# Performance work log

Hardware: AMD Instinct MI355X
Metric: run time of the kernel (lower is better)

Reference implementation:

```python
import jax, jax.numpy as jnp
import numpy as np

LRELU_SLOPE = 0.2  # PyG GATConv default negative_slope
LN_EPS = 1e-5


def _layer_norm(x, g, b):
    mu = x.mean(-1, keepdims=True)
    var = x.var(-1, keepdims=True)
    return (x - mu) / jnp.sqrt(var + LN_EPS) * g + b


def _gat_conv(x, src, dst, W, a_src, a_dst, bias, heads, out_c, concat):
    # PyG GATConv (eval mode, self-loops already appended to src/dst).
    N = x.shape[0]
    h = (x @ W).reshape(N, heads, out_c)            # [N,H,C]
    e_src = (h * a_src).sum(-1)                     # [N,H]
    e_dst = (h * a_dst).sum(-1)                     # [N,H]
    e = jax.nn.leaky_relu(e_src[src] + e_dst[dst], LRELU_SLOPE)  # [E,H]
    # segment softmax over incoming edges of each dst node
    m = jax.ops.segment_max(e, dst, num_segments=N)
    m = jnp.where(jnp.isfinite(m), m, 0.0)
    w = jnp.exp(e - m[dst])
    denom = jax.ops.segment_sum(w, dst, num_segments=N)
    alpha = w / (denom[dst] + 1e-16)                # [E,H]
    out = jax.ops.segment_sum(h[src] * alpha[:, :, None], dst, num_segments=N)  # [N,H,C]
    out = out.reshape(N, heads * out_c) if concat else out.mean(1)
    return out + bias


def setup_inputs() -> dict:
    key = jax.random.key(0)
    ks = jax.random.split(key, 16)
    N, E, F0, Hd, H, G = 50000, 800000, 32, 32, 4, 512
    s = 0.1
    nrm = lambda k, shape: jax.random.normal(k, shape, jnp.float32) * s
    d = {}
    d['x'] = jax.random.normal(ks[0], (N, F0), jnp.float32)
    d['edge_index'] = jax.random.randint(ks[1], (2, E), 0, N)
    d['batch'] = jnp.sort(jax.random.randint(ks[2], (N,), 0, G))
    d['num_graphs'] = G
    # layer 1: F0 -> (Hd, H heads, concat)
    d['W1'] = nrm(ks[3], (F0, H * Hd)); d['as1'] = nrm(ks[4], (H, Hd)); d['ad1'] = nrm(ks[5], (H, Hd))
    d['b1'] = jnp.zeros((H * Hd,)); d['g1'] = jnp.ones((H * Hd,)); d['be1'] = jnp.zeros((H * Hd,))
    # layer 2: H*Hd -> (Hd, H heads, concat)
    d['W2'] = nrm(ks[6], (H * Hd, H * Hd)); d['as2'] = nrm(ks[7], (H, Hd)); d['ad2'] = nrm(ks[8], (H, Hd))
    d['b2'] = jnp.zeros((H * Hd,)); d['g2'] = jnp.ones((H * Hd,)); d['be2'] = jnp.zeros((H * Hd,))
    # layer 3: H*Hd -> (Hd, 1 head, mean)
    d['W3'] = nrm(ks[9], (H * Hd, Hd)); d['as3'] = nrm(ks[10], (1, Hd)); d['ad3'] = nrm(ks[11], (1, Hd))
    d['b3'] = jnp.zeros((Hd,)); d['g3'] = jnp.ones((Hd,)); d['be3'] = jnp.zeros((Hd,))
    # classifier MLP: 2*Hd -> Hd -> Hd//2 -> 1 (torch Linear [out,in])
    d['cW1'] = nrm(ks[12], (Hd, 2 * Hd)); d['cb1'] = jnp.zeros((Hd,))
    d['cW2'] = nrm(ks[13], (Hd // 2, Hd)); d['cb2'] = jnp.zeros((Hd // 2,))
    d['cW3'] = nrm(ks[14], (1, Hd // 2)); d['cb3'] = jnp.zeros((1,))
    return d


def reference(x, edge_index, batch, num_graphs,
              W1, as1, ad1, b1, g1, be1,
              W2, as2, ad2, b2, g2, be2,
              W3, as3, ad3, b3, g3, be3,
              cW1, cb1, cW2, cb2, cW3, cb3):
    N = x.shape[0]
    loop = jnp.arange(N)
    src = jnp.concatenate([edge_index[0], loop])
    dst = jnp.concatenate([edge_index[1], loop])
    h = jax.nn.elu(_layer_norm(_gat_conv(x, src, dst, W1, as1, ad1, b1, 4, 32, True), g1, be1))
    h = jax.nn.elu(_layer_norm(_gat_conv(h, src, dst, W2, as2, ad2, b2, 4, 32, True), g2, be2))
    h = jax.nn.elu(_layer_norm(_gat_conv(h, src, dst, W3, as3, ad3, b3, 1, 32, False), g3, be3))
    cnt = jax.ops.segment_sum(jnp.ones((N,), h.dtype), batch, num_segments=num_graphs)
    x_mean = jax.ops.segment_sum(h, batch, num_segments=num_graphs) / jnp.maximum(cnt, 1.0)[:, None]
    x_max = jax.ops.segment_max(h, batch, num_segments=num_graphs)
    f = jnp.concatenate([x_mean, x_max], axis=1)        # [G, 64]
    f = jax.nn.relu(f @ cW1.T + cb1)
    f = jax.nn.relu(f @ cW2.T + cb2)
    return (f @ cW3.T + cb3).squeeze(-1)                 # [G]
```

## Files before the change

kernel.cpp:

```cpp
#include <hip/hip_runtime.h>
#include <hip/hip_fp16.h>
#include <math.h>

#define CDIV(a, b) (((a) + (b) - 1) / (b))
#define SCAN_BS 1024
#define NBUK 512
#define ATILE 4096

typedef _Float16 f16x8 __attribute__((ext_vector_type(8)));
typedef float f32x4 __attribute__((ext_vector_type(4)));

__device__ __forceinline__ unsigned encf(float v) {
    unsigned u = __float_as_uint(v);
    return (u & 0x80000000u) ? ~u : (u | 0x80000000u);
}
__device__ __forceinline__ float decf(unsigned k) {
    unsigned u = (k & 0x80000000u) ? (k ^ 0x80000000u) : ~k;
    return __uint_as_float(u);
}

__device__ __forceinline__ float lrelu(float v) {
    return v > 0.f ? v : 0.2f * v;
}

__global__ __launch_bounds__(256) void gemm_kernel(
    const float* __restrict__ X, const float* __restrict__ W,
    float* __restrict__ Y, int M, int K, int Nout) {
    int idx = blockIdx.x * blockDim.x + threadIdx.x;
    if (idx >= M * Nout) return;
    int row = idx / Nout;
    int col = idx - row * Nout;
    const float* xr = X + (size_t)row * K;
    const float* wc = W + col;
    float acc = 0.f;
    for (int k = 0; k < K; k += 4) {
        float4 xv = *(const float4*)(xr + k);
        acc += xv.x * wc[(size_t)(k + 0) * Nout];
        acc += xv.y * wc[(size_t)(k + 1) * Nout];
        acc += xv.z * wc[(size_t)(k + 2) * Nout];
        acc += xv.w * wc[(size_t)(k + 3) * Nout];
    }
    Y[idx] = acc;
}

__global__ __launch_bounds__(256) void wprep_kernel(
    const float* __restrict__ W, __half* __restrict__ Whf, int K, int NOUT) {
    int NK = K / 32, NT = NOUT / 16;
    int tot = NT * NK * 64;
    int idx = blockIdx.x * blockDim.x + threadIdx.x;
    if (idx >= tot) return;
    int l = idx & 63, f = idx >> 6;
    int ks = f % NK, t = f / NK;
    int quad = l >> 4, c15 = l & 15;
    _Float16 v[8];
#pragma unroll
    for (int j = 0; j < 8; ++j) {
        int k = ks * 32 + quad * 8 + j;
        int n = t * 16 + c15;
        v[j] = (_Float16)W[(size_t)k * NOUT + n];
    }
    *(uint4*)(Whf + (size_t)idx * 8) = *(uint4*)v;
}

__device__ __forceinline__ f16x8 loadA(const float* p) {
    float4 lo = *(const float4*)p;
    float4 hi = *(const float4*)(p + 4);
    f16x8 a;
    a[0] = (_Float16)lo.x; a[1] = (_Float16)lo.y;
    a[2] = (_Float16)lo.z; a[3] = (_Float16)lo.w;
    a[4] = (_Float16)hi.x; a[5] = (_Float16)hi.y;
    a[6] = (_Float16)hi.z; a[7] = (_Float16)hi.w;
    return a;
}
__device__ __forceinline__ f16x8 loadA(const __half* p) {
    return *(const f16x8*)p;
}

template <int K, int NOUT, typename XT>
__global__ __launch_bounds__(256) void gemm_mfma(
    const XT* __restrict__ X, const __half* __restrict__ Whf,
    __half* __restrict__ Y, int M) {
    constexpr int NK = K / 32, NT = NOUT / 16;
    int wave = threadIdx.x >> 6, lane = threadIdx.x & 63;
    int quad = lane >> 4, c15 = lane & 15;
    int row0 = (blockIdx.x * 4 + wave) * 16;
    if (row0 >= M) return;
    int arow = row0 + c15;
    if (arow >= M) arow = M - 1;
    const XT* xr = X + (size_t)arow * K + quad * 8;
    const f16x8* bp = (const f16x8*)Whf;
    f32x4 acc[NT];
#pragma unroll
    for (int t = 0; t < NT; ++t) {
        acc[t][0] = 0.f; acc[t][1] = 0.f; acc[t][2] = 0.f; acc[t][3] = 0.f;
    }
#pragma unroll
    for (int ks = 0; ks < NK; ++ks) {
        f16x8 a = loadA(xr + ks * 32);
#pragma unroll
        for (int t = 0; t < NT; ++t) {
            f16x8 b = bp[(t * NK + ks) * 64 + lane];
            acc[t] = __builtin_amdgcn_mfma_f32_16x16x32_f16(a, b, acc[t],
                                                            0, 0, 0);
        }
    }
#pragma unroll
    for (int r = 0; r < 4; ++r) {
        int row = row0 + quad * 4 + r;
        if (row < M) {
#pragma unroll
            for (int t = 0; t < NT; ++t)
                Y[(size_t)row * NOUT + t * 16 + c15] = (__half)acc[t][r];
        }
    }
}

__global__ __launch_bounds__(256) void attn16_kernel(
    const __half* __restrict__ h, const float* __restrict__ a_src,
    const float* __restrict__ a_dst, float* __restrict__ es,
    float* __restrict__ ed, int N, int H) {
    int idx = blockIdx.x * blockDim.x + threadIdx.x;
    if (idx >= N * H) return;
    int n = idx / H;
    int hh = idx - n * H;
    const __half* hp = h + (size_t)n * H * 32 + hh * 32;
    const float* ap = a_src + hh * 32;
    const float* bp = a_dst + hh * 32;
    float s = 0.f, d = 0.f;
#pragma unroll
    for (int c = 0; c < 32; c += 2) {
        float2 f = __half22float2(*(const __half2*)(hp + c));
        s += f.x * ap[c] + f.y * ap[c + 1];
        d += f.x * bp[c] + f.y * bp[c + 1];
    }
    es[idx] = s;
    ed[idx] = d;
}

__global__ __launch_bounds__(256) void attn_kernel(
    const float* __restrict__ h, const float* __restrict__ a_src,
    const float* __restrict__ a_dst, float* __restrict__ es,
    float* __restrict__ ed, int N, int H, int C) {
    int idx = blockIdx.x * blockDim.x + threadIdx.x;
    if (idx >= N * H) return;
    int n = idx / H;
    int hh = idx - n * H;
    const float* hp = h + (size_t)n * H * C + (size_t)hh * C;
    const float* ap = a_src + hh * C;
    const float* bp = a_dst + hh * C;
    float s = 0.f, d = 0.f;
    for (int c = 0; c < C; c += 4) {
        float4 hv = *(const float4*)(hp + c);
        float4 av = *(const float4*)(ap + c);
        float4 bv = *(const float4*)(bp + c);
        s += hv.x * av.x + hv.y * av.y + hv.z * av.z + hv.w * av.w;
        d += hv.x * bv.x + hv.y * bv.y + hv.z * bv.z + hv.w * bv.w;
    }
    es[idx] = s;
    ed[idx] = d;
}

__global__ __launch_bounds__(256) void binA1_kernel(
    const int* __restrict__ ei, int E, int* __restrict__ ghist) {
    __shared__ int lh[NBUK];
    int t = threadIdx.x;
    for (int i = t; i < NBUK; i += 256) lh[i] = 0;
    __syncthreads();
    int base = blockIdx.x * ATILE;
#pragma unroll 4
    for (int j = 0; j < ATILE / 256; ++j) {
        int idx = base + t + 256 * j;
        if (idx < E) atomicAdd(&lh[ei[E + idx] >> 7], 1);
    }
    __syncthreads();
    int* gh = ghist + (size_t)blockIdx.x * NBUK;
    for (int i = t; i < NBUK; i += 256) gh[i] = lh[i];
}

__global__ __launch_bounds__(64) void binA2a_kernel(
    int* __restrict__ ghist, int* __restrict__ tot, int nblk) {
    int b = blockIdx.x;
    int lane = threadIdx.x;
    int accb = 0;
    for (int chunk = 0; chunk < nblk; chunk += 64) {
        int i = chunk + lane;
        int v = (i < nblk) ? ghist[(size_t)i * NBUK + b] : 0;
        int s = v;
        for (int off = 1; off < 64; off <<= 1) {
            int tv = __shfl_up(s, off);
            if (lane >= off) s += tv;
        }
        if (i < nblk) ghist[(size_t)i * NBUK + b] = s - v + accb;
        accb += __shfl(s, 63);
    }
    if (lane == 0) tot[b] = accb;
}

__global__ __launch_bounds__(NBUK) void binA2b_kernel(
    const int* __restrict__ tot, int* __restrict__ bucketptr,
    int* __restrict__ rowptr, int N, int E) {
    __shared__ int sc[NBUK];
    int b = threadIdx.x;
    int v = tot[b];
    sc[b] = v;
    __syncthreads();
    for (int off = 1; off < NBUK; off <<= 1) {
        int t = (b >= off) ? sc[b - off] : 0;
        __syncthreads();
        sc[b] += t;
        __syncthreads();
    }
    bucketptr[b] = sc[b] - v;
    if (b == 0) {
        bucketptr[NBUK] = E;
        rowptr[N] = E + N;
    }
}

__global__ __launch_bounds__(256) void binA3_kernel(
    const int* __restrict__ ei, int E, const int* __restrict__ ghist,
    const int* __restrict__ bucketptr, unsigned* __restrict__ ebuf) {
    __shared__ int lcur[NBUK];
    int t = threadIdx.x;
    const int* gh = ghist + (size_t)blockIdx.x * NBUK;
    for (int i = t; i < NBUK; i += 256) lcur[i] = gh[i] + bucketptr[i];
    __syncthreads();
    int base = blockIdx.x * ATILE;
#pragma unroll 4
    for (int j = 0; j < ATILE / 256; ++j) {
        int idx = base + t + 256 * j;
        if (idx < E) {
            int s = ei[idx];
            int d = ei[E + idx];
            int pos = atomicAdd(&lcur[d >> 7], 1);
            ebuf[pos] = ((unsigned)d << 16) | (unsigned)s;
        }
    }
}

__global__ __launch_bounds__(256) void binB_kernel(
    const unsigned* __restrict__ ebuf, const int* __restrict__ bucketptr,
    int* __restrict__ rowptr, int* __restrict__ csrc, int N) {
    __shared__ int cnt_[128];
    __shared__ int pre[128];
    __shared__ int lcur[128];
    int b = blockIdx.x;
    int t = threadIdx.x;
    int n0 = b << 7;
    if (t < 128) cnt_[t] = 0;
    __syncthreads();
    int beg = bucketptr[b], end = bucketptr[b + 1];
    for (int i = beg + t; i < end; i += 256)
        atomicAdd(&cnt_[(ebuf[i] >> 16) - n0], 1);
    __syncthreads();
    if (t < 128) pre[t] = (n0 + t < N) ? (cnt_[t] + 1) : 0;
    __syncthreads();
    for (int off = 1; off < 128; off <<= 1) {
        int v = 0;
        if (t < 128 && t >= off) v = pre[t - off];
        __syncthreads();
        if (t < 128) pre[t] += v;
        __syncthreads();
    }
    int cbase = beg + n0;
    if (t < 128 && n0 + t < N) {
        int excl = pre[t] - (cnt_[t] + 1);
        int rp = cbase + excl;
        rowptr[n0 + t] = rp;
        csrc[rp] = n0 + t;
        lcur[t] = rp + 1;
    }
    __syncthreads();
    for (int i = beg + t; i < end; i += 256) {
        unsigned e = ebuf[i];
        int d = (int)(e >> 16) - n0;
        int s = (int)(e & 0xFFFFu);
        int pos = atomicAdd(&lcur[d], 1);
        csrc[pos] = s;
    }
}

__global__ __launch_bounds__(256) void deg_kernel(const int* __restrict__ ei,
                                                  int E,
                                                  int* __restrict__ deg) {
    int e = blockIdx.x * blockDim.x + threadIdx.x;
    if (e >= E) return;
    atomicAdd(&deg[ei[E + e]], 1);
}

__global__ __launch_bounds__(SCAN_BS) void scan1_kernel(
    const int* __restrict__ deg, int* __restrict__ rowptr,
    int* __restrict__ bsum, int N) {
    __shared__ int tmp[SCAN_BS];
    int tid = threadIdx.x;
    int gid = blockIdx.x * SCAN_BS + tid;
    int v = (gid < N) ? (deg[gid] + 1) : 0;
    tmp[tid] = v;
    __syncthreads();
    for (int off = 1; off < SCAN_BS; off <<= 1) {
        int t = (tid >= off) ? tmp[tid - off] : 0;
        __syncthreads();
        tmp[tid] += t;
        __syncthreads();
    }
    if (gid < N) rowptr[gid] = tmp[tid] - v;
    if (tid == SCAN_BS - 1) bsum[blockIdx.x] = tmp[tid];
}

__global__ void scan2_kernel(int* __restrict__ bsum, int nb) {
    if (threadIdx.x == 0 && blockIdx.x == 0) {
        int acc = 0;
        for (int i = 0; i < nb; ++i) {
            int t = bsum[i];
            bsum[i] = acc;
            acc += t;
        }
    }
}

__global__ __launch_bounds__(SCAN_BS) void scan3_kernel(
    int* __restrict__ rowptr, int* __restrict__ cursor,
    int* __restrict__ csrc, const int* __restrict__ bsum, int N, int total) {
    int gid = blockIdx.x * SCAN_BS + threadIdx.x;
    if (gid < N) {
        int v = rowptr[gid] + bsum[blockIdx.x];
        rowptr[gid] = v;
        cursor[gid] = v + 1;
        csrc[v] = gid;
    }
    if (gid == 0) rowptr[N] = total;
}

__global__ __launch_bounds__(256) void scatter_kernel(
    const int* __restrict__ ei, int E, int* __restrict__ cursor,
    int* __restrict__ csrc) {
    int e = blockIdx.x * blockDim.x + threadIdx.x;
    if (e >= E) return;
    int s = ei[e];
    int d = ei[E + e];
    int pos = atomicAdd(&cursor[d], 1);
    csrc[pos] = s;
}

__global__ __launch_bounds__(256) void aggr_ln128_kernel(
    const int* __restrict__ rowptr, const int* __restrict__ csrc,
    const __half* __restrict__ h, const float* __restrict__ es,
    const float* __restrict__ ed, const float* __restrict__ bias,
    const float* __restrict__ gam, const float* __restrict__ bet,
    __half* __restrict__ outp, int N) {
    constexpr int D = 128, H = 4;
    int wave = (blockIdx.x * blockDim.x + threadIdx.x) >> 6;
    int lane = threadIdx.x & 63;
    int grp = lane >> 5;
    int li = lane & 31;
    int d = wave * 2 + grp;
    if (d >= N) return;
    int c = li * 4;
    int hh = li >> 3;
    float edv = ed[d * H + hh];
    float l = 0.f;
    float ax = 0.f, ay = 0.f, az = 0.f, aw = 0.f;
    int k = rowptr[d], end = rowptr[d + 1];
    for (; k + 8 <= end; k += 8) {
        int s[8];
#pragma unroll
        for (int j = 0; j < 8; ++j) s[j] = csrc[k + j];
        float e[8];
#pragma unroll
        for (int j = 0; j < 8; ++j) e[j] = es[s[j] * H + hh];
        uint2 u[8];
#pragma unroll
        for (int j = 0; j < 8; ++j)
            u[j] = *(const uint2*)(h + (size_t)s[j] * D + c);
#pragma unroll
        for (int j = 0; j < 8; ++j) {
            float w = __expf(lrelu(e[j] + edv));
            float2 f0 = __half22float2(*(__half2*)&u[j].x);
            float2 f1 = __half22float2(*(__half2*)&u[j].y);
            l += w;
            ax += w * f0.x; ay += w * f0.y; az += w * f1.x; aw += w * f1.y;
        }
    }
    for (; k + 4 <= end; k += 4) {
        int s[4];
#pragma unroll
        for (int j = 0; j < 4; ++j) s[j] = csrc[k + j];
        float e[4];
#pragma unroll
        for (int j = 0; j < 4; ++j) e[j] = es[s[j] * H + hh];
        uint2 u[4];
#pragma unroll
        for (int j = 0; j < 4; ++j)
            u[j] = *(const uint2*)(h + (size_t)s[j] * D + c);
#pragma unroll
        for (int j = 0; j < 4; ++j) {
            float w = __expf(lrelu(e[j] + edv));
            float2 f0 = __half22float2(*(__half2*)&u[j].x);
            float2 f1 = __half22float2(*(__half2*)&u[j].y);
            l += w;
            ax += w * f0.x; ay += w * f0.y; az += w * f1.x; aw += w * f1.y;
        }
    }
    for (; k < end; ++k) {
        int s = csrc[k];
        float w = __expf(lrelu(es[s * H + hh] + edv));
        uint2 u = *(const uint2*)(h + (size_t)s * D + c);
        float2 f0 = __half22float2(*(__half2*)&u.x);
        float2 f1 = __half22float2(*(__half2*)&u.y);
        l += w;
        ax += w * f0.x; ay += w * f0.y; az += w * f1.x; aw += w * f1.y;
    }
    float rl = 1.f / (l + 1e-16f);
    float4 b4 = *(const float4*)(bias + c);
    float v0 = ax * rl + b4.x;
    float v1 = ay * rl + b4.y;
    float v2 = az * rl + b4.z;
    float v3 = aw * rl + b4.w;
    float s = v0 + v1 + v2 + v3;
    float ss = v0 * v0 + v1 * v1 + v2 * v2 + v3 * v3;
    for (int off = 16; off; off >>= 1) {
        s += __shfl_xor(s, off);
        ss += __shfl_xor(ss, off);
    }
    float mean = s / D;
    float var = ss / D - mean * mean;
    float rstd = rsqrtf(var + 1e-5f);
    float4 g4 = *(const float4*)(gam + c);
    float4 t4 = *(const float4*)(bet + c);
    float4 o;
    o.x = (v0 - mean) * rstd * g4.x + t4.x;
    o.y = (v1 - mean) * rstd * g4.y + t4.y;
    o.z = (v2 - mean) * rstd * g4.z + t4.z;
    o.w = (v3 - mean) * rstd * g4.w + t4.w;
    o.x = o.x > 0.f ? o.x : expm1f(o.x);
    o.y = o.y > 0.f ? o.y : expm1f(o.y);
    o.z = o.z > 0.f ? o.z : expm1f(o.z);
    o.w = o.w > 0.f ? o.w : expm1f(o.w);
    __half2 p0 = __floats2half2_rn(o.x, o.y);
    __half2 p1 = __floats2half2_rn(o.z, o.w);
    uint2 u;
    u.x = *(unsigned*)&p0;
    u.y = *(unsigned*)&p1;
    *(uint2*)(outp + (size_t)d * D + c) = u;
}

__global__ __launch_bounds__(256) void aggr_ln32_pool_kernel(
    const int* __restrict__ rowptr, const int* __restrict__ csrc,
    const __half* __restrict__ h, const float* __restrict__ es,
    const float* __restrict__ ed, const float* __restrict__ bias,
    const float* __restrict__ gam, const float* __restrict__ bet,
    const int* __restrict__ batch, float* __restrict__ psum,
    unsigned* __restrict__ pmax, float* __restrict__ cnt, int N) {
    constexpr int D = 32;
    __shared__ float lsum[2][32];
    __shared__ unsigned lmax[2][32];
    __shared__ float lcnt[2];
    __shared__ int g0s;
    int tid = threadIdx.x;
    int wave = (blockIdx.x * blockDim.x + tid) >> 6;
    int lane = tid & 63;
    int half = lane >> 5;
    int c = lane & 31;
    int d = wave * 2 + half;
    int dbase = blockIdx.x * 8;
    if (tid < 64) {
        lsum[tid >> 5][tid & 31] = 0.f;
        lmax[tid >> 5][tid & 31] = 0u;
    }
    if (tid < 2) lcnt[tid] = 0.f;
    if (tid == 0) g0s = batch[dbase < N ? dbase : (N - 1)];
    __syncthreads();
    int g0 = g0s;
    bool active = d < N;
    if (active) {
        float edv = ed[d];
        float l = 0.f, acc = 0.f;
        int k = rowptr[d], end = rowptr[d + 1];
        for (; k + 8 <= end; k += 8) {
            int s[8];
#pragma unroll
            for (int j = 0; j < 8; ++j) s[j] = csrc[k + j];
            float e[8];
#pragma unroll
            for (int j = 0; j < 8; ++j) e[j] = es[s[j]];
            float hv[8];
#pragma unroll
            for (int j = 0; j < 8; ++j)
                hv[j] = __half2float(h[(size_t)s[j] * D + c]);
#pragma unroll
            for (int j = 0; j < 8; ++j) {
                float w = __expf(lrelu(e[j] + edv));
                l += w;
                acc += w * hv[j];
            }
        }
        for (; k + 4 <= end; k += 4) {
            int s[4];
#pragma unroll
            for (int j = 0; j < 4; ++j) s[j] = csrc[k + j];
            float e[4];
#pragma unroll
            for (int j = 0; j < 4; ++j) e[j] = es[s[j]];
            float hv[4];
#pragma unroll
            for (int j = 0; j < 4; ++j)
                hv[j] = __half2float(h[(size_t)s[j] * D + c]);
#pragma unroll
            for (int j = 0; j < 4; ++j) {
                float w = __expf(lrelu(e[j] + edv));
                l += w;
                acc += w * hv[j];
            }
        }
        for (; k < end; ++k) {
            int s = csrc[k];
            float w = __expf(lrelu(es[s] + edv));
            l += w;
            acc += w * __half2float(h[(size_t)s * D + c]);
        }
        float v = acc / (l + 1e-16f) + bias[c];
        float sm = v, ss = v * v;
        for (int off = 16; off; off >>= 1) {
            sm += __shfl_xor(sm, off);
            ss += __shfl_xor(ss, off);
        }
        float mean = sm / D;
        float var = ss / D - mean * mean;
        float rstd = rsqrtf(var + 1e-5f);
        float o = (v - mean) * rstd * gam[c] + bet[c];
        o = o > 0.f ? o : expm1f(o);
        int g = batch[d];
        int goff = g - g0;
        if (goff >= 0 && goff < 2) {
            atomicAdd(&lsum[goff][c], o);
            atomicMax(&lmax[goff][c], encf(o));
            if (c == 0) atomicAdd(&lcnt[goff], 1.0f);
        } else {
            atomicAdd(&psum[g * D + c], o);
            atomicMax(&pmax[g * D + c], encf(o));
            if (c == 0) atomicAdd(&cnt[g], 1.0f);
        }
    }
    __syncthreads();
    if (tid < 64) {
        int go = tid >> 5, cc = tid & 31;
        unsigned m = lmax[go][cc];
        if (m != 0u) {
            int gg = g0 + go;
            atomicAdd(&psum[gg * D + cc], lsum[go][cc]);
            atomicMax(&pmax[gg * D + cc], m);
            if (cc == 0) atomicAdd(&cnt[gg], lcnt[go]);
        }
    }
}

__global__ __launch_bounds__(256) void aggr_csr_kernel(
    const int* __restrict__ rowptr, const int* __restrict__ csrc,
    const float* __restrict__ h, const float* __restrict__ es,
    const float* __restrict__ ed, float* __restrict__ outp, int N, int H,
    int C) {
    int D = H * C;
    int wave = (blockIdx.x * blockDim.x + threadIdx.x) >> 6;
    int lane = threadIdx.x & 63;
    if (wave >= N) return;
    int d = wave;
    int c0 = lane, c1 = lane + 64;
    bool a0 = c0 < D, a1 = c1 < D;
    int h0 = a0 ? c0 / C : 0;
    int h1 = a1 ? c1 / C : 0;
    float edv0 = a0 ? ed[d * H + h0] : 0.f;
    float edv1 = a1 ? ed[d * H + h1] : 0.f;
    float m0 = -INFINITY, m1 = -INFINITY;
    float l0 = 0.f, l1 = 0.f, acc0 = 0.f, acc1 = 0.f;
    int beg = rowptr[d], end = rowptr[d + 1];
    for (int k = beg; k < end; ++k) {
        int s = csrc[k];
        const float* hp = h + (size_t)s * D;
        if (a0) {
            float v = lrelu(es[s * H + h0] + edv0);
            float nm = fmaxf(m0, v);
            float sc = __expf(m0 - nm);
            float w = __expf(v - nm);
            l0 = l0 * sc + w;
            acc0 = acc0 * sc + w * hp[c0];
            m0 = nm;
        }
        if (a1) {
            float v = lrelu(es[s * H + h1] + edv1);
            float nm = fmaxf(m1, v);
            float sc = __expf(m1 - nm);
            float w = __expf(v - nm);
            l1 = l1 * sc + w;
            acc1 = acc1 * sc + w * hp[c1];
            m1 = nm;
        }
    }
    if (a0) outp[(size_t)d * D + c0] = acc0 / (l0 + 1e-16f);
    if (a1) outp[(size_t)d * D + c1] = acc1 / (l1 + 1e-16f);
}

__global__ __launch_bounds__(64) void ln_elu_kernel(
    const float* __restrict__ in, const float* __restrict__ bias,
    const float* __restrict__ gam, const float* __restrict__ bet,
    float* __restrict__ outp, int D) {
    int n = blockIdx.x;
    int lane = threadIdx.x;
    int c0 = lane, c1 = lane + 64;
    bool a0 = c0 < D, a1 = c1 < D;
    float v0 = 0.f, v1 = 0.f;
    if (a0) v0 = in[(size_t)n * D + c0] + bias[c0];
    if (a1) v1 = in[(size_t)n * D + c1] + bias[c1];
    float s = v0 + v1;
    float ss = v0 * v0 + v1 * v1;
    for (int off = 32; off; off >>= 1) {
        s += __shfl_xor(s, off);
        ss += __shfl_xor(ss, off);
    }
    float mean = s / D;
    float var = ss / D - mean * mean;
    float rstd = rsqrtf(var + 1e-5f);
    if (a0) {
        float o = (v0 - mean) * rstd * gam[c0] + bet[c0];
        outp[(size_t)n * D + c0] = o > 0.f ? o : expm1f(o);
    }
    if (a1) {
        float o = (v1 - mean) * rstd * gam[c1] + bet[c1];
        outp[(size_t)n * D + c1] = o > 0.f ? o : expm1f(o);
    }
}

__global__ __launch_bounds__(256) void pool_kernel(
    const float* __restrict__ h, const int* __restrict__ batch, int N, int C,
    float* __restrict__ psum, unsigned* __restrict__ pmax,
    float* __restrict__ cnt) {
    int idx = blockIdx.x * blockDim.x + threadIdx.x;
    if (idx >= N * C) return;
    int n = idx / C;
    int c = idx - n * C;
    int g = batch[n];
    float v = h[(size_t)n * C + c];
    atomicAdd(&psum[g * C + c], v);
    atomicMax(&pmax[g * C + c], encf(v));
    if (c == 0) atomicAdd(&cnt[g], 1.0f);
}

__global__ __launch_bounds__(64) void mlp_kernel(
    const float* __restrict__ psum, const unsigned* __restrict__ pmax,
    const float* __restrict__ cnt, const float* __restrict__ cW1,
    const float* __restrict__ cb1, const float* __restrict__ cW2,
    const float* __restrict__ cb2, const float* __restrict__ cW3,
    const float* __restrict__ cb3, float* __restrict__ outp, int C) {
    __shared__ float f[64];
    __shared__ float t1[32];
    __shared__ float t2[16];
    int g = blockIdx.x;
    int t = threadIdx.x;
    float c = fmaxf(cnt[g], 1.0f);
    if (t < C) {
        f[t] = psum[g * C + t] / c;
    } else if (t < 2 * C) {
        unsigned k = pmax[g * C + (t - C)];
        f[t] = (k == 0u) ? -INFINITY : decf(k);
    }
    __syncthreads();
    if (t < 32) {
        float a = cb1[t];
        for (int i = 0; i < 64; ++i) a += f[i] * cW1[t * 64 + i];
        t1[t] = fmaxf(a, 0.f);
    }
    __syncthreads();
    if (t < 16) {
        float a = cb2[t];
        for (int i = 0; i < 32; ++i) a += t1[i] * cW2[t * 32 + i];
        t2[t] = fmaxf(a, 0.f);
    }
    __syncthreads();
    if (t == 0) {
        float a = cb3[0];
        for (int i = 0; i < 16; ++i) a += t2[i] * cW3[i];
        outp[g] = a;
    }
}

extern "C" void kernel_launch(void* const* d_in, const int* in_sizes, int n_in,
                              void* d_out, int out_size, void* d_ws,
                              size_t ws_size, hipStream_t stream) {
    const float* x = (const float*)d_in[0];
    const int* ei = (const int*)d_in[1];
    const int* batch = (const int*)d_in[2];
    const float* W1 = (const float*)d_in[4];
    const float* as1 = (const float*)d_in[5];
    const float* ad1 = (const float*)d_in[6];
    const float* b1 = (const float*)d_in[7];
    const float* g1 = (const float*)d_in[8];
    const float* be1 = (const float*)d_in[9];
    const float* W2 = (const float*)d_in[10];
    const float* as2 = (const float*)d_in[11];
    const float* ad2 = (const float*)d_in[12];
    const float* b2 = (const float*)d_in[13];
    const float* g2 = (const float*)d_in[14];
    const float* be2 = (const float*)d_in[15];
    const float* W3 = (const float*)d_in[16];
    const float* as3 = (const float*)d_in[17];
    const float* ad3 = (const float*)d_in[18];
    const float* b3 = (const float*)d_in[19];
    const float* g3 = (const float*)d_in[20];
    const float* be3 = (const float*)d_in[21];
    const float* cW1 = (const float*)d_in[22];
    const float* cb1 = (const float*)d_in[23];
    const float* cW2 = (const float*)d_in[24];
    const float* cb2 = (const float*)d_in[25];
    const float* cW3 = (const float*)d_in[26];
    const float* cb3 = (const float*)d_in[27];

    const int N = in_sizes[2];
    const int E = in_sizes[1] / 2;
    const int F0 = in_sizes[0] / N;
    const int Hd = in_sizes[19];
    const int H = in_sizes[5] / Hd;
    const int D = H * Hd;
    const int H3 = in_sizes[17] / Hd;
    const int G = out_size;
    const int EN = E + N;
    const bool shapes_ok = (F0 == 32 && Hd == 32 && H == 4 && D == 128 &&
                            H3 == 1 && N <= 65536);

    char* w = (char*)d_ws;
    size_t off = 0;
    auto carve = [&](size_t bytes) -> void* {
        void* p = w + off;
        off = (off + bytes + 255) & ~(size_t)255;
        return p;
    };
    float* Q = (float*)carve((size_t)N * D * 4);
    __half* Qh = (__half*)Q;
    float* R = (float*)carve((size_t)N * D * 4);
    float* P = (float*)carve((size_t)N * D * 4);
    __half* Ph = (__half*)P;
    float* es = (float*)carve((size_t)N * H * 4);
    float* ed = (float*)carve((size_t)N * H * 4);
    int* rowptr = (int*)carve((size_t)(N + 1) * 4);
    int* cursor = (int*)carve((size_t)N * 4);
    int* csrc = (int*)carve((size_t)EN * 4);
    int* bsum = (int*)carve((size_t)CDIV(N, SCAN_BS) * 4);
    const int nblkA = CDIV(E, ATILE);
    int* ghist = (int*)carve((size_t)nblkA * NBUK * 4);
    int* tot = (int*)carve((size_t)NBUK * 4);
    int* bucketptr = (int*)carve((size_t)(NBUK + 1) * 4);
    unsigned* ebuf = (unsigned*)carve((size_t)E * 4);
    __half* wh1 = (__half*)carve((size_t)8 * 1 * 64 * 8 * 2);
    __half* wh2 = (__half*)carve((size_t)8 * 4 * 64 * 8 * 2);
    __half* wh3 = (__half*)carve((size_t)2 * 4 * 64 * 8 * 2);
    float* psum = (float*)carve((size_t)G * Hd * 4);
    unsigned* pmax = (unsigned*)carve((size_t)G * Hd * 4);
    float* cnt = (float*)carve((size_t)G * 4);
    (void)ws_size;
    (void)n_in;

    const int BLK = 256;
    const int nb = CDIV(N, SCAN_BS);

    hipMemsetAsync(psum, 0, (size_t)G * Hd * 4, stream);
    hipMemsetAsync(pmax, 0, (size_t)G * Hd * 4, stream);
    hipMemsetAsync(cnt, 0, (size_t)G * 4, stream);

    if (shapes_ok) {
        binA1_kernel<<<nblkA, 256, 0, stream>>>(ei, E, ghist);
        binA2a_kernel<<<NBUK, 64, 0, stream>>>(ghist, tot, nblkA);
        binA2b_kernel<<<1, NBUK, 0, stream>>>(tot, bucketptr, rowptr, N, E);
        binA3_kernel<<<nblkA, 256, 0, stream>>>(ei, E, ghist, bucketptr, ebuf);
        binB_kernel<<<CDIV(N, 128), 256, 0, stream>>>(ebuf, bucketptr, rowptr,
                                                      csrc, N);
        wprep_kernel<<<CDIV(8 * 1 * 64, BLK), BLK, 0, stream>>>(W1, wh1, 32, 128);
        wprep_kernel<<<CDIV(8 * 4 * 64, BLK), BLK, 0, stream>>>(W2, wh2, 128, 128);
        wprep_kernel<<<CDIV(2 * 4 * 64, BLK), BLK, 0, stream>>>(W3, wh3, 128, 32);
        gemm_mfma<32, 128, float><<<CDIV(N, 64), 256, 0, stream>>>(x, wh1, Qh, N);
        attn16_kernel<<<CDIV(N * 4, BLK), BLK, 0, stream>>>(Qh, as1, ad1, es, ed, N, 4);
        aggr_ln128_kernel<<<CDIV(N, 8), 256, 0, stream>>>(
            rowptr, csrc, Qh, es, ed, b1, g1, be1, Ph, N);
        gemm_mfma<128, 128, __half><<<CDIV(N, 64), 256, 0, stream>>>(Ph, wh2, Qh, N);
        attn16_kernel<<<CDIV(N * 4, BLK), BLK, 0, stream>>>(Qh, as2, ad2, es, ed, N, 4);
        aggr_ln128_kernel<<<CDIV(N, 8), 256, 0, stream>>>(
            rowptr, csrc, Qh, es, ed, b2, g2, be2, Ph, N);
        gemm_mfma<128, 32, __half><<<CDIV(N, 64), 256, 0, stream>>>(Ph, wh3, Qh, N);
        attn16_kernel<<<CDIV(N, BLK), BLK, 0, stream>>>(Qh, as3, ad3, es, ed, N, 1);
        aggr_ln32_pool_kernel<<<CDIV(N, 8), 256, 0, stream>>>(
            rowptr, csrc, Qh, es, ed, b3, g3, be3, batch, psum, pmax, cnt, N);
    } else {
        hipMemsetAsync(cursor, 0, (size_t)N * 4, stream);
        deg_kernel<<<CDIV(E, BLK), BLK, 0, stream>>>(ei, E, cursor);
        scan1_kernel<<<nb, SCAN_BS, 0, stream>>>(cursor, rowptr, bsum, N);
        scan2_kernel<<<1, 64, 0, stream>>>(bsum, nb);
        scan3_kernel<<<nb, SCAN_BS, 0, stream>>>(rowptr, cursor, csrc, bsum, N, EN);
        scatter_kernel<<<CDIV(E, BLK), BLK, 0, stream>>>(ei, E, cursor, csrc);
        gemm_kernel<<<CDIV(N * D, BLK), BLK, 0, stream>>>(x, W1, Q, N, F0, D);
        attn_kernel<<<CDIV(N * H, BLK), BLK, 0, stream>>>(Q, as1, ad1, es, ed, N, H, Hd);
        aggr_csr_kernel<<<CDIV(N, 4), BLK, 0, stream>>>(rowptr, csrc, Q, es, ed, R, N, H, Hd);
        ln_elu_kernel<<<N, 64, 0, stream>>>(R, b1, g1, be1, P, D);
        gemm_kernel<<<CDIV(N * D, BLK), BLK, 0, stream>>>(P, W2, Q, N, D, D);
        attn_kernel<<<CDIV(N * H, BLK), BLK, 0, stream>>>(Q, as2, ad2, es, ed, N, H, Hd);
        aggr_csr_kernel<<<CDIV(N, 4), BLK, 0, stream>>>(rowptr, csrc, Q, es, ed, R, N, H, Hd);
        ln_elu_kernel<<<N, 64, 0, stream>>>(R, b2, g2, be2, P, D);
        gemm_kernel<<<CDIV(N * Hd, BLK), BLK, 0, stream>>>(P, W3, Q, N, D, Hd);
        attn_kernel<<<CDIV(N * H3, BLK), BLK, 0, stream>>>(Q, as3, ad3, es, ed, N, H3, Hd);
        aggr_csr_kernel<<<CDIV(N, 4), BLK, 0, stream>>>(rowptr, csrc, Q, es, ed, R, N, H3, Hd);
        ln_elu_kernel<<<N, 64, 0, stream>>>(R, b3, g3, be3, P, Hd);
        pool_kernel<<<CDIV(N * Hd, BLK), BLK, 0, stream>>>(P, batch, N, Hd, psum, pmax, cnt);
    }

    mlp_kernel<<<G, 64, 0, stream>>>(psum, pmax, cnt, cW1, cb1, cW2, cb2, cW3,
                                     cb3, (float*)d_out, Hd);
}
```

Baseline: 316.9 us.

## Fuse attention logits into MFMA GEMM and merge small setup kernels

The per-node attention score computation (es/ed) moves into the GEMM epilogue, using cross-lane shuffles on the accumulator registers. This drops three separate attention kernels and their re-read of the fp16 features. The single-block bucket scan is folded into binA3 and binB, which each recompute it, and the three weight-prep launches become one kernel. Zeroing of the pooling buffers moves into binA1 instead of three memsets, cutting launch count at the cost of some redundant per-block scan work and the assumption that psum/pmax/cnt are laid out contiguously.

```diff
diff --git a/kernel.cpp b/kernel.cpp
--- a/kernel.cpp
+++ b/kernel.cpp
@@ -43,23 +43,37 @@
     Y[idx] = acc;
 }
 
-__global__ __launch_bounds__(256) void wprep_kernel(
-    const float* __restrict__ W, __half* __restrict__ Whf, int K, int NOUT) {
-    int NK = K / 32, NT = NOUT / 16;
-    int tot = NT * NK * 64;
-    int idx = blockIdx.x * blockDim.x + threadIdx.x;
-    if (idx >= tot) return;
+__device__ __forceinline__ void wprep_one(const float* __restrict__ W,
+                                          __half* __restrict__ Whf, int K,
+                                          int NOUT, int idx) {
+    int NK = K / 32;
     int l = idx & 63, f = idx >> 6;
-    int ks = f % NK, t = f / NK;
+    int ks = f % NK, tt = f / NK;
     int quad = l >> 4, c15 = l & 15;
     _Float16 v[8];
 #pragma unroll
     for (int j = 0; j < 8; ++j) {
         int k = ks * 32 + quad * 8 + j;
-        int n = t * 16 + c15;
+        int n = tt * 16 + c15;
         v[j] = (_Float16)W[(size_t)k * NOUT + n];
     }
     *(uint4*)(Whf + (size_t)idx * 8) = *(uint4*)v;
+}
+
+__global__ __launch_bounds__(256) void wprep_all_kernel(
+    const float* __restrict__ W1, const float* __restrict__ W2,
+    const float* __restrict__ W3, __half* __restrict__ wh1,
+    __half* __restrict__ wh2, __half* __restrict__ wh3,
+    int* __restrict__ rowptr, int N, int E) {
+    int idx = blockIdx.x * 256 + threadIdx.x;
+    if (idx == 0) rowptr[N] = E + N;
+    if (idx < 512) {
+        wprep_one(W1, wh1, 32, 128, idx);
+    } else if (idx < 2560) {
+        wprep_one(W2, wh2, 128, 128, idx - 512);
+    } else if (idx < 3072) {
+        wprep_one(W3, wh3, 128, 32, idx - 2560);
+    }
 }
 
 __device__ __forceinline__ f16x8 loadA(const float* p) {
@@ -76,11 +90,14 @@
     return *(const f16x8*)p;
 }
 
-template <int K, int NOUT, typename XT>
-__global__ __launch_bounds__(256) void gemm_mfma(
+template <int K, int NOUT, int HH, typename XT>
+__global__ __launch_bounds__(256) void gemm_mfma_attn(
     const XT* __restrict__ X, const __half* __restrict__ Whf,
-    __half* __restrict__ Y, int M) {
+    __half* __restrict__ Y, const float* __restrict__ a_src,
+    const float* __restrict__ a_dst, float* __restrict__ es,
+    float* __restrict__ ed, int M) {
     constexpr int NK = K / 32, NT = NOUT / 16;
+    static_assert(NT == 2 * HH, "32 channels per head assumed");
     int wave = threadIdx.x >> 6, lane = threadIdx.x & 63;
     int quad = lane >> 4, c15 = lane & 15;
     int row0 = (blockIdx.x * 4 + wave) * 16;
@@ -113,28 +130,162 @@
                 Y[(size_t)row * NOUT + t * 16 + c15] = (__half)acc[t][r];
         }
     }
-}
-
-__global__ __launch_bounds__(256) void attn16_kernel(
-    const __half* __restrict__ h, const float* __restrict__ a_src,
-    const float* __restrict__ a_dst, float* __restrict__ es,
-    float* __restrict__ ed, int N, int H) {
-    int idx = blockIdx.x * blockDim.x + threadIdx.x;
-    if (idx >= N * H) return;
-    int n = idx / H;
-    int hh = idx - n * H;
-    const __half* hp = h + (size_t)n * H * 32 + hh * 32;
-    const float* ap = a_src + hh * 32;
-    const float* bp = a_dst + hh * 32;
-    float s = 0.f, d = 0.f;
-#pragma unroll
-    for (int c = 0; c < 32; c += 2) {
-        float2 f = __half22float2(*(const __half2*)(hp + c));
-        s += f.x * ap[c] + f.y * ap[c + 1];
-        d += f.x * bp[c] + f.y * bp[c + 1];
-    }
-    es[idx] = s;
-    ed[idx] = d;
+    float asv[NT], adv[NT];
+#pragma unroll
+    for (int t = 0; t < NT; ++t) {
+        asv[t] = a_src[t * 16 + c15];
+        adv[t] = a_dst[t * 16 + c15];
+    }
+#pragma unroll
+    for (int h = 0; h < HH; ++h) {
+#pragma unroll
+        for (int r = 0; r < 4; ++r) {
+            float s = acc[2 * h][r] * asv[2 * h] +
+                      acc[2 * h + 1][r] * asv[2 * h + 1];
+            float dd = acc[2 * h][r] * adv[2 * h] +
+                       acc[2 * h + 1][r] * adv[2 * h + 1];
+#pragma unroll
+            for (int off = 8; off >= 1; off >>= 1) {
+                s += __shfl_xor(s, off);
+                dd += __shfl_xor(dd, off);
+            }
+            int row = row0 + quad * 4 + r;
+            if (row < M) {
+                if (c15 == 0) es[row * HH + h] = s;
+                if (c15 == 1) ed[row * HH + h] = dd;
+            }
+        }
+    }
+}
+
+__global__ __launch_bounds__(256) void binA1_kernel(
+    const int* __restrict__ ei, int E, int* __restrict__ ghist,
+    int* __restrict__ pool0, int poolN) {
+    __shared__ int lh[NBUK];
+    int t = threadIdx.x;
+    int gid = blockIdx.x * 256 + t;
+    if (gid < poolN) pool0[gid] = 0;
+    for (int i = t; i < NBUK; i += 256) lh[i] = 0;
+    __syncthreads();
+    int base = blockIdx.x * ATILE;
+#pragma unroll 4
+    for (int j = 0; j < ATILE / 256; ++j) {
+        int idx = base + t + 256 * j;
+        if (idx < E) atomicAdd(&lh[ei[E + idx] >> 7], 1);
+    }
+    __syncthreads();
+    int* gh = ghist + (size_t)blockIdx.x * NBUK;
+    for (int i = t; i < NBUK; i += 256) gh[i] = lh[i];
+}
+
+__global__ __launch_bounds__(64) void binA2a_kernel(
+    int* __restrict__ ghist, int* __restrict__ tot, int nblk) {
+    int b = blockIdx.x;
+    int lane = threadIdx.x;
+    int accb = 0;
+    for (int chunk = 0; chunk < nblk; chunk += 64) {
+        int i = chunk + lane;
+        int v = (i < nblk) ? ghist[(size_t)i * NBUK + b] : 0;
+        int s = v;
+        for (int off = 1; off < 64; off <<= 1) {
+            int tv = __shfl_up(s, off);
+            if (lane >= off) s += tv;
+        }
+        if (i < nblk) ghist[(size_t)i * NBUK + b] = s - v + accb;
+        accb += __shfl(s, 63);
+    }
+    if (lane == 0) tot[b] = accb;
+}
+
+__device__ __forceinline__ void bucketScan(const int* __restrict__ tot,
+                                           int* __restrict__ sc, int t,
+                                           int& a0, int& a1, int& excl) {
+    a0 = tot[2 * t];
+    a1 = tot[2 * t + 1];
+    int pair = a0 + a1;
+    sc[t] = pair;
+    __syncthreads();
+#pragma unroll
+    for (int off = 1; off < 256; off <<= 1) {
+        int v = (t >= off) ? sc[t - off] : 0;
+        __syncthreads();
+        sc[t] += v;
+        __syncthreads();
+    }
+    excl = sc[t] - pair;
+}
+
+__global__ __launch_bounds__(256) void binA3_kernel(
+    const int* __restrict__ ei, int E, const int* __restrict__ ghist,
+    const int* __restrict__ tot, unsigned* __restrict__ ebuf) {
+    __shared__ int lcur[NBUK];
+    __shared__ int sc[256];
+    int t = threadIdx.x;
+    int a0, a1, excl;
+    bucketScan(tot, sc, t, a0, a1, excl);
+    const int* gh = ghist + (size_t)blockIdx.x * NBUK;
+    lcur[2 * t] = gh[2 * t] + excl;
+    lcur[2 * t + 1] = gh[2 * t + 1] + excl + a0;
+    __syncthreads();
+    int base = blockIdx.x * ATILE;
+#pragma unroll 4
+    for (int j = 0; j < ATILE / 256; ++j) {
+        int idx = base + t + 256 * j;
+        if (idx < E) {
+            int s = ei[idx];
+            int d = ei[E + idx];
+            int pos = atomicAdd(&lcur[d >> 7], 1);
+            ebuf[pos] = ((unsigned)d << 16) | (unsigned)s;
+        }
+    }
+}
+
+__global__ __launch_bounds__(256) void binB_kernel(
+    const unsigned* __restrict__ ebuf, const int* __restrict__ tot,
+    int* __restrict__ rowptr, int* __restrict__ csrc, int N) {
+    __shared__ int cnt_[128];
+    __shared__ int pre[128];
+    __shared__ int lcur[128];
+    __shared__ int sc[256];
+    __shared__ int begS;
+    int b = blockIdx.x;
+    int t = threadIdx.x;
+    int n0 = b << 7;
+    int totb = tot[b];
+    if (t < 128) cnt_[t] = 0;
+    int a0, a1, excl;
+    bucketScan(tot, sc, t, a0, a1, excl);
+    if (t == (b >> 1)) begS = (b & 1) ? (excl + a0) : excl;
+    __syncthreads();
+    int beg = begS, end = begS + totb;
+    for (int i = beg + t; i < end; i += 256)
+        atomicAdd(&cnt_[(ebuf[i] >> 16) - n0], 1);
+    __syncthreads();
+    if (t < 128) pre[t] = (n0 + t < N) ? (cnt_[t] + 1) : 0;
+    __syncthreads();
+    for (int off = 1; off < 128; off <<= 1) {
+        int v = 0;
+        if (t < 128 && t >= off) v = pre[t - off];
+        __syncthreads();
+        if (t < 128) pre[t] += v;
+        __syncthreads();
+    }
+    int cbase = beg + n0;
+    if (t < 128 && n0 + t < N) {
+        int ex = pre[t] - (cnt_[t] + 1);
+        int rp = cbase + ex;
+        rowptr[n0 + t] = rp;
+        csrc[rp] = n0 + t;
+        lcur[t] = rp + 1;
+    }
+    __syncthreads();
+    for (int i = beg + t; i < end; i += 256) {
+        unsigned e = ebuf[i];
+        int d = (int)(e >> 16) - n0;
+        int s = (int)(e & 0xFFFFu);
+        int pos = atomicAdd(&lcur[d], 1);
+        csrc[pos] = s;
+    }
 }
 
 __global__ __launch_bounds__(256) void attn_kernel(
@@ -158,126 +309,6 @@
     }
     es[idx] = s;
     ed[idx] = d;
-}
-
-__global__ __launch_bounds__(256) void binA1_kernel(
-    const int* __restrict__ ei, int E, int* __restrict__ ghist) {
-    __shared__ int lh[NBUK];
-    int t = threadIdx.x;
-    for (int i = t; i < NBUK; i += 256) lh[i] = 0;
-    __syncthreads();
-    int base = blockIdx.x * ATILE;
-#pragma unroll 4
-    for (int j = 0; j < ATILE / 256; ++j) {
-        int idx = base + t + 256 * j;
-        if (idx < E) atomicAdd(&lh[ei[E + idx] >> 7], 1);
-    }
-    __syncthreads();
-    int* gh = ghist + (size_t)blockIdx.x * NBUK;
-    for (int i = t; i < NBUK; i += 256) gh[i] = lh[i];
-}
-
-__global__ __launch_bounds__(64) void binA2a_kernel(
-    int* __restrict__ ghist, int* __restrict__ tot, int nblk) {
-    int b = blockIdx.x;
-    int lane = threadIdx.x;
-    int accb = 0;
-    for (int chunk = 0; chunk < nblk; chunk += 64) {
-        int i = chunk + lane;
-        int v = (i < nblk) ? ghist[(size_t)i * NBUK + b] : 0;
-        int s = v;
-        for (int off = 1; off < 64; off <<= 1) {
-            int tv = __shfl_up(s, off);
-            if (lane >= off) s += tv;
-        }
-        if (i < nblk) ghist[(size_t)i * NBUK + b] = s - v + accb;
-        accb += __shfl(s, 63);
-    }
-    if (lane == 0) tot[b] = accb;
-}
-
-__global__ __launch_bounds__(NBUK) void binA2b_kernel(
-    const int* __restrict__ tot, int* __restrict__ bucketptr,
-    int* __restrict__ rowptr, int N, int E) {
-    __shared__ int sc[NBUK];
-    int b = threadIdx.x;
-    int v = tot[b];
-    sc[b] = v;
-    __syncthreads();
-    for (int off = 1; off < NBUK; off <<= 1) {
-        int t = (b >= off) ? sc[b - off] : 0;
-        __syncthreads();
-        sc[b] += t;
-        __syncthreads();
-    }
-    bucketptr[b] = sc[b] - v;
-    if (b == 0) {
-        bucketptr[NBUK] = E;
-        rowptr[N] = E + N;
-    }
-}
-
-__global__ __launch_bounds__(256) void binA3_kernel(
-    const int* __restrict__ ei, int E, const int* __restrict__ ghist,
-    const int* __restrict__ bucketptr, unsigned* __restrict__ ebuf) {
-    __shared__ int lcur[NBUK];
-    int t = threadIdx.x;
-    const int* gh = ghist + (size_t)blockIdx.x * NBUK;
-    for (int i = t; i < NBUK; i += 256) lcur[i] = gh[i] + bucketptr[i];
-    __syncthreads();
-    int base = blockIdx.x * ATILE;
-#pragma unroll 4
-    for (int j = 0; j < ATILE / 256; ++j) {
-        int idx = base + t + 256 * j;
-        if (idx < E) {
-            int s = ei[idx];
-            int d = ei[E + idx];
-            int pos = atomicAdd(&lcur[d >> 7], 1);
-            ebuf[pos] = ((unsigned)d << 16) | (unsigned)s;
-        }
-    }
-}
-
-__global__ __launch_bounds__(256) void binB_kernel(
-    const unsigned* __restrict__ ebuf, const int* __restrict__ bucketptr,
-    int* __restrict__ rowptr, int* __restrict__ csrc, int N) {
-    __shared__ int cnt_[128];
-    __shared__ int pre[128];
-    __shared__ int lcur[128];
-    int b = blockIdx.x;
-    int t = threadIdx.x;
-    int n0 = b << 7;
-    if (t < 128) cnt_[t] = 0;
-    __syncthreads();
-    int beg = bucketptr[b], end = bucketptr[b + 1];
-    for (int i = beg + t; i < end; i += 256)
-        atomicAdd(&cnt_[(ebuf[i] >> 16) - n0], 1);
-    __syncthreads();
-    if (t < 128) pre[t] = (n0 + t < N) ? (cnt_[t] + 1) : 0;
-    __syncthreads();
-    for (int off = 1; off < 128; off <<= 1) {
-        int v = 0;
-        if (t < 128 && t >= off) v = pre[t - off];
-        __syncthreads();
-        if (t < 128) pre[t] += v;
-        __syncthreads();
-    }
-    int cbase = beg + n0;
-    if (t < 128 && n0 + t < N) {
-        int excl = pre[t] - (cnt_[t] + 1);
-        int rp = cbase + excl;
-        rowptr[n0 + t] = rp;
-        csrc[rp] = n0 + t;
-        lcur[t] = rp + 1;
-    }
-    __syncthreads();
-    for (int i = beg + t; i < end; i += 256) {
-        unsigned e = ebuf[i];
-        int d = (int)(e >> 16) - n0;
-        int s = (int)(e & 0xFFFFu);
-        int pos = atomicAdd(&lcur[d], 1);
-        csrc[pos] = s;
-    }
 }
 
 __global__ __launch_bounds__(256) void deg_kernel(const int* __restrict__ ei,
@@ -746,7 +777,6 @@
     const int nblkA = CDIV(E, ATILE);
     int* ghist = (int*)carve((size_t)nblkA * NBUK * 4);
     int* tot = (int*)carve((size_t)NBUK * 4);
-    int* bucketptr = (int*)carve((size_t)(NBUK + 1) * 4);
     unsigned* ebuf = (unsigned*)carve((size_t)E * 4);
     __half* wh1 = (__half*)carve((size_t)8 * 1 * 64 * 8 * 2);
     __half* wh2 = (__half*)carve((size_t)8 * 4 * 64 * 8 * 2);
@@ -759,34 +789,33 @@
 
     const int BLK = 256;
     const int nb = CDIV(N, SCAN_BS);
-
-    hipMemsetAsync(psum, 0, (size_t)G * Hd * 4, stream);
-    hipMemsetAsync(pmax, 0, (size_t)G * Hd * 4, stream);
-    hipMemsetAsync(cnt, 0, (size_t)G * 4, stream);
+    const int poolInts = G * Hd * 2 + G;
 
     if (shapes_ok) {
-        binA1_kernel<<<nblkA, 256, 0, stream>>>(ei, E, ghist);
+        binA1_kernel<<<nblkA, 256, 0, stream>>>(ei, E, ghist, (int*)psum,
+                                                poolInts);
         binA2a_kernel<<<NBUK, 64, 0, stream>>>(ghist, tot, nblkA);
-        binA2b_kernel<<<1, NBUK, 0, stream>>>(tot, bucketptr, rowptr, N, E);
-        binA3_kernel<<<nblkA, 256, 0, stream>>>(ei, E, ghist, bucketptr, ebuf);
-        binB_kernel<<<CDIV(N, 128), 256, 0, stream>>>(ebuf, bucketptr, rowptr,
+        binA3_kernel<<<nblkA, 256, 0, stream>>>(ei, E, ghist, tot, ebuf);
+        binB_kernel<<<CDIV(N, 128), 256, 0, stream>>>(ebuf, tot, rowptr,
                                                       csrc, N);
-        wprep_kernel<<<CDIV(8 * 1 * 64, BLK), BLK, 0, stream>>>(W1, wh1, 32, 128);
-        wprep_kernel<<<CDIV(8 * 4 * 64, BLK), BLK, 0, stream>>>(W2, wh2, 128, 128);
-        wprep_kernel<<<CDIV(2 * 4 * 64, BLK), BLK, 0, stream>>>(W3, wh3, 128, 32);
-        gemm_mfma<32, 128, float><<<CDIV(N, 64), 256, 0, stream>>>(x, wh1, Qh, N);
-        attn16_kernel<<<CDIV(N * 4, BLK), BLK, 0, stream>>>(Qh, as1, ad1, es, ed, N, 4);
+        wprep_all_kernel<<<12, 256, 0, stream>>>(W1, W2, W3, wh1, wh2, wh3,
+                                                 rowptr, N, E);
+        gemm_mfma_attn<32, 128, 4, float><<<CDIV(N, 64), 256, 0, stream>>>(
+            x, wh1, Qh, as1, ad1, es, ed, N);
         aggr_ln128_kernel<<<CDIV(N, 8), 256, 0, stream>>>(
             rowptr, csrc, Qh, es, ed, b1, g1, be1, Ph, N);
-        gemm_mfma<128, 128, __half><<<CDIV(N, 64), 256, 0, stream>>>(Ph, wh2, Qh, N);
-        attn16_kernel<<<CDIV(N * 4, BLK), BLK, 0, stream>>>(Qh, as2, ad2, es, ed, N, 4);
+        gemm_mfma_attn<128, 128, 4, __half><<<CDIV(N, 64), 256, 0, stream>>>(
+            Ph, wh2, Qh, as2, ad2, es, ed, N);
         aggr_ln128_kernel<<<CDIV(N, 8), 256, 0, stream>>>(
             rowptr, csrc, Qh, es, ed, b2, g2, be2, Ph, N);
-        gemm_mfma<128, 32, __half><<<CDIV(N, 64), 256, 0, stream>>>(Ph, wh3, Qh, N);
-        attn16_kernel<<<CDIV(N, BLK), BLK, 0, stream>>>(Qh, as3, ad3, es, ed, N, 1);
+        gemm_mfma_attn<128, 32, 1, __half><<<CDIV(N, 64), 256, 0, stream>>>(
+            Ph, wh3, Qh, as3, ad3, es, ed, N);
         aggr_ln32_pool_kernel<<<CDIV(N, 8), 256, 0, stream>>>(
             rowptr, csrc, Qh, es, ed, b3, g3, be3, batch, psum, pmax, cnt, N);
     } else {
+        hipMemsetAsync(psum, 0, (size_t)G * Hd * 4, stream);
+        hipMemsetAsync(pmax, 0, (size_t)G * Hd * 4, stream);
+        hipMemsetAsync(cnt, 0, (size_t)G * 4, stream);
         hipMemsetAsync(cursor, 0, (size_t)N * 4, stream);
         deg_kernel<<<CDIV(E, BLK), BLK, 0, stream>>>(ei, E, cursor);
         scan1_kernel<<<nb, SCAN_BS, 0, stream>>>(cursor, rowptr, bsum, N);
```

Measured after the change: 295.4 us. 6.8% less time.
